# Kernel tuning notes

Measured on AMD Instinct MI355X. Metric: run time of the kernel, lower is better.

## Reference

```python
import jax, jax.numpy as jnp
import numpy as np

ALPHA = 0.2  # LeakyReLU negative slope


def setup_inputs() -> dict:
    key = jax.random.key(0)
    k1, k2, k3, k4 = jax.random.split(key, 4)
    N, E, F_IN, F_OUT = 100000, 1600000, 128, 32
    x = jax.random.normal(k1, (N, F_IN), dtype=jnp.float32)
    W = jax.random.normal(k2, (F_IN, F_OUT), dtype=jnp.float32) * 0.1
    a = jax.random.normal(k3, (2 * F_OUT, 1), dtype=jnp.float32) * 0.1
    edge_index = jax.random.randint(k4, (2, E), 0, N, dtype=jnp.int64)
    return {"x": x, "W": W, "a": a, "edge_index": edge_index}


def reference(x, W, a, edge_index):
    N = x.shape[0]
    F_OUT = W.shape[1]
    Wx = x @ W  # [N, F_OUT]
    src = edge_index[0]  # row indices (softmax groups)
    dst = edge_index[1]
    # e = leakyrelu([Wx_i || Wx_j] @ a); split a to avoid materializing the concat
    a_src = a[:F_OUT, 0]
    a_dst = a[F_OUT:, 0]
    e = (Wx @ a_src)[src] + (Wx @ a_dst)[dst]  # [E]
    e = jnp.where(e >= 0, e, ALPHA * e)
    # sparse softmax over rows (src)
    m = jax.ops.segment_max(e, src, num_segments=N)  # -inf for empty rows
    m = jnp.where(jnp.isinf(m), 0.0, m)
    exp_v = jnp.exp(e - m[src])
    s = jax.ops.segment_sum(exp_v, src, num_segments=N)
    s = jnp.where(s == 0, 1.0, s)
    att = exp_v / s[src]  # [E]
    # sparse matmul: h[i] = sum_j att[i,j] * Wx[j]
    h = jax.ops.segment_sum(att[:, None] * Wx[dst], src, num_segments=N)
    return jax.nn.elu(h)
```

## Files before the change

kernel.cpp:

```cpp
#include <hip/hip_runtime.h>
#include <hip/hip_bf16.h>
#include <math.h>

#define ALPHA 0.2f
#define F_IN 128
#define F_OUT 32
#define BSHIFT 9
#define BNODES 512
#define DSTBITS 17
#define CHUNK 4096
#define SLABCAP 16384

typedef __attribute__((ext_vector_type(8))) short short8;
typedef __attribute__((ext_vector_type(4))) float float4v;

__device__ __forceinline__ short f2bf(float f) {
    __hip_bfloat16 h = __float2bfloat16(f);
    return __builtin_bit_cast(short, h);
}
__device__ __forceinline__ float bf2f(unsigned short u) {
    return __uint_as_float((unsigned)u << 16);
}

__global__ __launch_bounds__(256) void k_phaseA(
    const float* __restrict__ x, const float* __restrict__ W,
    const float* __restrict__ a, unsigned short* __restrict__ Wxh,
    float* __restrict__ s1, float* __restrict__ s2, int nTiles, int N, int nT1,
    const int* __restrict__ src, const int* __restrict__ dst,
    int* __restrict__ bcur, unsigned* __restrict__ packed, int E)
{
    if ((int)blockIdx.x < nT1) {
        __shared__ short Wt[32 * 136];
        for (int i = threadIdx.x; i < F_IN * F_OUT; i += 256) {
            int k = i >> 5, n = i & 31;
            Wt[n * 136 + k] = f2bf(W[i]);
        }
        __syncthreads();

        int wave = threadIdx.x >> 6;
        int lane = threadIdx.x & 63;
        int tile = blockIdx.x * 4 + wave;
        if (tile >= nTiles) return;

        int m    = lane & 15;
        int quad = lane >> 4;
        int row  = tile * 16 + m;
        int rowc = row < N ? row : N - 1;

        short8 bf[2][4];
#pragma unroll
        for (int t = 0; t < 2; ++t)
#pragma unroll
            for (int s = 0; s < 4; ++s)
                bf[t][s] = *(const short8*)&Wt[(t * 16 + m) * 136 + s * 32 + quad * 8];

        float4v acc0 = {0.f, 0.f, 0.f, 0.f};
        float4v acc1 = {0.f, 0.f, 0.f, 0.f};
        const float* xr = x + (size_t)rowc * F_IN + quad * 8;
#pragma unroll
        for (int s = 0; s < 4; ++s) {
            float4 xa = *(const float4*)(xr + s * 32);
            float4 xb = *(const float4*)(xr + s * 32 + 4);
            short8 af;
            af[0] = f2bf(xa.x); af[1] = f2bf(xa.y); af[2] = f2bf(xa.z); af[3] = f2bf(xa.w);
            af[4] = f2bf(xb.x); af[5] = f2bf(xb.y); af[6] = f2bf(xb.z); af[7] = f2bf(xb.w);
            acc0 = __builtin_amdgcn_mfma_f32_16x16x32_bf16(af, bf[0][s], acc0, 0, 0, 0);
            acc1 = __builtin_amdgcn_mfma_f32_16x16x32_bf16(af, bf[1][s], acc1, 0, 0, 0);
        }

        int rbase = tile * 16 + quad * 4;
#pragma unroll
        for (int r = 0; r < 4; ++r) {
            if (rbase + r < N) {
                Wxh[(size_t)(rbase + r) * F_OUT + m]      = (unsigned short)f2bf(acc0[r]);
                Wxh[(size_t)(rbase + r) * F_OUT + m + 16] = (unsigned short)f2bf(acc1[r]);
            }
        }

        float a1c0 = a[m], a1c1 = a[m + 16];
        float a2c0 = a[F_OUT + m], a2c1 = a[F_OUT + m + 16];
#pragma unroll
        for (int r = 0; r < 4; ++r) {
            float v1 = acc0[r] * a1c0 + acc1[r] * a1c1;
            float v2 = acc0[r] * a2c0 + acc1[r] * a2c1;
#pragma unroll
            for (int off = 8; off >= 1; off >>= 1) {
                v1 += __shfl_xor(v1, off, 16);
                v2 += __shfl_xor(v2, off, 16);
            }
            if (m == 0 && rbase + r < N) {
                s1[rbase + r] = v1;
                s2[rbase + r] = v2;
            }
        }
    } else {
        __shared__ int hist[256];
        __shared__ int cur[256];
        int t = threadIdx.x;
        hist[t] = 0;
        __syncthreads();
        int e0 = ((int)blockIdx.x - nT1) * CHUNK;
        int sreg[16], dreg[16];
#pragma unroll
        for (int k = 0; k < 4; ++k) {
            int e = e0 + k * 1024 + t * 4;
            int4 s4, d4;
            if (e + 3 < E) {
                s4 = *(const int4*)&src[e];
                d4 = *(const int4*)&dst[e];
            } else {
                s4.x = (e + 0 < E) ? src[e + 0] : -1;
                s4.y = (e + 1 < E) ? src[e + 1] : -1;
                s4.z = (e + 2 < E) ? src[e + 2] : -1;
                s4.w = (e + 3 < E) ? src[e + 3] : -1;
                d4.x = (e + 0 < E) ? dst[e + 0] : 0;
                d4.y = (e + 1 < E) ? dst[e + 1] : 0;
                d4.z = (e + 2 < E) ? dst[e + 2] : 0;
                d4.w = (e + 3 < E) ? dst[e + 3] : 0;
            }
            sreg[k * 4 + 0] = s4.x; dreg[k * 4 + 0] = d4.x;
            sreg[k * 4 + 1] = s4.y; dreg[k * 4 + 1] = d4.y;
            sreg[k * 4 + 2] = s4.z; dreg[k * 4 + 2] = d4.z;
            sreg[k * 4 + 3] = s4.w; dreg[k * 4 + 3] = d4.w;
        }
#pragma unroll
        for (int k = 0; k < 16; ++k)
            if (sreg[k] >= 0) atomicAdd(&hist[sreg[k] >> BSHIFT], 1);
        __syncthreads();
        if (hist[t] > 0) cur[t] = atomicAdd(&bcur[t], hist[t]);
        __syncthreads();
#pragma unroll
        for (int k = 0; k < 16; ++k) {
            if (sreg[k] >= 0) {
                int b = sreg[k] >> BSHIFT;
                int p = atomicAdd(&cur[b], 1);
                if (p < SLABCAP)
                    packed[(size_t)b * SLABCAP + p] =
                        ((unsigned)(sreg[k] & (BNODES - 1)) << DSTBITS) | (unsigned)dreg[k];
            }
        }
    }
}

__global__ __launch_bounds__(256) void k_finalize(
    const unsigned* __restrict__ packed, const int* __restrict__ bcnt,
    int* __restrict__ counts, int* __restrict__ row_ptr,
    int* __restrict__ dst_sorted, int N, int NBK)
{
    __shared__ int hist[BNODES];
    __shared__ int psum[256];
    __shared__ int cur[BNODES];
    int b = blockIdx.x;
    int t = threadIdx.x;

    psum[t] = (t < b) ? min(bcnt[t], SLABCAP) : 0;
    __syncthreads();
    for (int off = 128; off >= 1; off >>= 1) {
        if (t < off) psum[t] += psum[t + off];
        __syncthreads();
    }
    int e0 = psum[0];
    __syncthreads();

    int cnt = min(bcnt[b], SLABCAP);
    const unsigned* pb = packed + (size_t)b * SLABCAP;

    hist[t] = 0; hist[t + 256] = 0;
    __syncthreads();
    for (int e = t; e < cnt; e += 256)
        atomicAdd(&hist[pb[e] >> DSTBITS], 1);
    __syncthreads();
    int a0 = hist[2 * t], a1 = hist[2 * t + 1];
    psum[t] = a0 + a1;
    __syncthreads();
    for (int off = 1; off < 256; off <<= 1) {
        int v = (t >= off) ? psum[t - off] : 0;
        __syncthreads();
        psum[t] += v;
        __syncthreads();
    }
    int excl = (t > 0) ? psum[t - 1] : 0;
    int p0 = e0 + excl;
    int p1 = p0 + a0;
    cur[2 * t] = p0;
    cur[2 * t + 1] = p1;
    int n0 = b << BSHIFT;
    if (n0 + 2 * t < N)     { counts[n0 + 2 * t] = a0;     row_ptr[n0 + 2 * t] = p0; }
    if (n0 + 2 * t + 1 < N) { counts[n0 + 2 * t + 1] = a1; row_ptr[n0 + 2 * t + 1] = p1; }
    __syncthreads();
    for (int e = t; e < cnt; e += 256) {
        unsigned v = pb[e];
        int p = atomicAdd(&cur[v >> DSTBITS], 1);
        dst_sorted[p] = v & ((1u << DSTBITS) - 1);
    }
}

__global__ __launch_bounds__(256) void k_node(
    const int* __restrict__ row_ptr, const int* __restrict__ counts,
    const int* __restrict__ dst_s,
    const float* __restrict__ s1, const float* __restrict__ s2,
    const unsigned short* __restrict__ Wxh, float* __restrict__ out, int N)
{
    int g = threadIdx.x >> 5;
    int l = threadIdx.x & 31;
    int n = blockIdx.x * 8 + g;
    if (n >= N) return;

    int base = row_ptr[n];
    int deg  = counts[n];
    float s1n = s1[n];
    int es = l >> 3;
    int fl = l & 7;

    float4 acc = {0.f, 0.f, 0.f, 0.f};
    float sum = 0.f;
    for (int j0 = 0; j0 < deg; j0 += 32) {
        int j = j0 + l;
        int   d_l = 0;
        float p_l = 0.f;
        if (j < deg) {
            d_l = dst_s[base + j];
            float ev = s1n + s2[d_l];
            ev = ev >= 0.f ? ev : ALPHA * ev;
            p_l = expf(ev);
        }
        sum += p_l;
        int cnt = min(32, deg - j0);
        int nIter = (cnt + 3) >> 2;
        for (int t = 0; t < nIter; ++t) {
            int e = t * 4 + es;
            float p = __shfl(p_l, e, 32);
            int   d = __shfl(d_l, e, 32);
            ushort4 w = *(const ushort4*)&Wxh[(size_t)d * F_OUT + fl * 4];
            acc.x += p * bf2f(w.x);
            acc.y += p * bf2f(w.y);
            acc.z += p * bf2f(w.z);
            acc.w += p * bf2f(w.w);
        }
    }
#pragma unroll
    for (int off = 8; off <= 16; off <<= 1) {
        acc.x += __shfl_xor(acc.x, off, 32);
        acc.y += __shfl_xor(acc.y, off, 32);
        acc.z += __shfl_xor(acc.z, off, 32);
        acc.w += __shfl_xor(acc.w, off, 32);
    }
#pragma unroll
    for (int off = 16; off >= 1; off >>= 1)
        sum += __shfl_xor(sum, off, 32);

    if (es == 0) {
        float inv = (deg > 0) ? 1.f / sum : 0.f;
        float4 h;
        h.x = acc.x * inv; h.y = acc.y * inv; h.z = acc.z * inv; h.w = acc.w * inv;
        h.x = h.x > 0.f ? h.x : expm1f(h.x);
        h.y = h.y > 0.f ? h.y : expm1f(h.y);
        h.z = h.z > 0.f ? h.z : expm1f(h.z);
        h.w = h.w > 0.f ? h.w : expm1f(h.w);
        *(float4*)&out[(size_t)n * F_OUT + fl * 4] = h;
    }
}

extern "C" void kernel_launch(void* const* d_in, const int* in_sizes, int n_in,
                              void* d_out, int out_size, void* d_ws, size_t ws_size,
                              hipStream_t stream)
{
    const float* x = (const float*)d_in[0];
    const float* W = (const float*)d_in[1];
    const float* a = (const float*)d_in[2];
    const int*  ei = (const int*)d_in[3];

    int N = in_sizes[0] / F_IN;
    int E = in_sizes[3] / 2;
    const int* src = ei;
    const int* dst = ei + E;
    int NBK = (N + BNODES - 1) >> BSHIFT;
    int nTiles = (N + 15) / 16;
    int nT1 = (nTiles + 3) / 4;
    int nEB = (E + CHUNK - 1) / CHUNK;

    unsigned short* Wxh = (unsigned short*)d_ws;
    float*    s1       = (float*)d_ws + (size_t)16 * N;
    float*    s2       = s1 + N;
    int*      counts   = (int*)(s2 + N);
    int*      row_ptr  = counts + N;
    int*      bcur     = row_ptr + N;
    unsigned* packed   = (unsigned*)(bcur + 256);
    int*      dst_sorted = (int*)(packed + (size_t)NBK * SLABCAP);

    float* out = (float*)d_out;

    hipMemsetAsync(bcur, 0, 256 * 4, stream);

    k_phaseA<<<nT1 + nEB, 256, 0, stream>>>(x, W, a, Wxh, s1, s2, nTiles, N, nT1,
                                            src, dst, bcur, packed, E);
    k_finalize<<<NBK, 256, 0, stream>>>(packed, bcur, counts, row_ptr, dst_sorted, N, NBK);
    k_node<<<(N + 7) / 8, 256, 0, stream>>>(row_ptr, counts, dst_sorted, s1, s2, Wxh, out, N);
}
```

Measured before the change: 170.6 us.

## Fuse CSR finalize and node aggregation into per-bucket LDS atomic accumulation

Shrinks source buckets from 512 to 64 nodes, which gives about 1563 buckets, and drops the finalize pass that built row_ptr and dst_sorted. A single per-bucket kernel now reads the packed edges straight from each slab, computes the exp weights, and accumulates the softmax denominator and the weighted Wx rows into shared memory with float atomics. This removes one kernel launch and a full global scatter/sort pass. In exchange it relies on contended LDS atomics, and the slab capacity of 2048 per 64-node bucket risks silently dropping edges for high-degree buckets. It also skips max-subtraction in the softmax, as the code before already did.

```diff
diff --git a/kernel.cpp b/kernel.cpp
--- a/kernel.cpp
+++ b/kernel.cpp
@@ -5,11 +5,13 @@
 #define ALPHA 0.2f
 #define F_IN 128
 #define F_OUT 32
-#define BSHIFT 9
-#define BNODES 512
+#define BSHIFT 6
+#define BNODES 64
 #define DSTBITS 17
 #define CHUNK 4096
-#define SLABCAP 16384
+#define SLABCAP 2048
+#define NBKMAX 1600
+#define ACCSTRIDE 33
 
 typedef __attribute__((ext_vector_type(8))) short short8;
 typedef __attribute__((ext_vector_type(4))) float float4v;
@@ -27,7 +29,7 @@
     const float* __restrict__ a, unsigned short* __restrict__ Wxh,
     float* __restrict__ s1, float* __restrict__ s2, int nTiles, int N, int nT1,
     const int* __restrict__ src, const int* __restrict__ dst,
-    int* __restrict__ bcur, unsigned* __restrict__ packed, int E)
+    int* __restrict__ bcur, unsigned* __restrict__ packed, int E, int NBK)
 {
     if ((int)blockIdx.x < nT1) {
         __shared__ short Wt[32 * 136];
@@ -94,10 +96,10 @@
             }
         }
     } else {
-        __shared__ int hist[256];
-        __shared__ int cur[256];
+        __shared__ int hist[NBKMAX];
+        __shared__ int cur[NBKMAX];
         int t = threadIdx.x;
-        hist[t] = 0;
+        for (int i = t; i < NBK; i += 256) hist[i] = 0;
         __syncthreads();
         int e0 = ((int)blockIdx.x - nT1) * CHUNK;
         int sreg[16], dreg[16];
@@ -127,7 +129,8 @@
         for (int k = 0; k < 16; ++k)
             if (sreg[k] >= 0) atomicAdd(&hist[sreg[k] >> BSHIFT], 1);
         __syncthreads();
-        if (hist[t] > 0) cur[t] = atomicAdd(&bcur[t], hist[t]);
+        for (int i = t; i < NBK; i += 256)
+            if (hist[i] > 0) cur[i] = atomicAdd(&bcur[i], hist[i]);
         __syncthreads();
 #pragma unroll
         for (int k = 0; k < 16; ++k) {
@@ -142,122 +145,80 @@
     }
 }
 
-__global__ __launch_bounds__(256) void k_finalize(
+__global__ __launch_bounds__(256) void k_bnode(
     const unsigned* __restrict__ packed, const int* __restrict__ bcnt,
-    int* __restrict__ counts, int* __restrict__ row_ptr,
-    int* __restrict__ dst_sorted, int N, int NBK)
-{
-    __shared__ int hist[BNODES];
-    __shared__ int psum[256];
-    __shared__ int cur[BNODES];
-    int b = blockIdx.x;
-    int t = threadIdx.x;
-
-    psum[t] = (t < b) ? min(bcnt[t], SLABCAP) : 0;
-    __syncthreads();
-    for (int off = 128; off >= 1; off >>= 1) {
-        if (t < off) psum[t] += psum[t + off];
-        __syncthreads();
-    }
-    int e0 = psum[0];
-    __syncthreads();
-
-    int cnt = min(bcnt[b], SLABCAP);
-    const unsigned* pb = packed + (size_t)b * SLABCAP;
-
-    hist[t] = 0; hist[t + 256] = 0;
-    __syncthreads();
-    for (int e = t; e < cnt; e += 256)
-        atomicAdd(&hist[pb[e] >> DSTBITS], 1);
-    __syncthreads();
-    int a0 = hist[2 * t], a1 = hist[2 * t + 1];
-    psum[t] = a0 + a1;
-    __syncthreads();
-    for (int off = 1; off < 256; off <<= 1) {
-        int v = (t >= off) ? psum[t - off] : 0;
-        __syncthreads();
-        psum[t] += v;
-        __syncthreads();
-    }
-    int excl = (t > 0) ? psum[t - 1] : 0;
-    int p0 = e0 + excl;
-    int p1 = p0 + a0;
-    cur[2 * t] = p0;
-    cur[2 * t + 1] = p1;
-    int n0 = b << BSHIFT;
-    if (n0 + 2 * t < N)     { counts[n0 + 2 * t] = a0;     row_ptr[n0 + 2 * t] = p0; }
-    if (n0 + 2 * t + 1 < N) { counts[n0 + 2 * t + 1] = a1; row_ptr[n0 + 2 * t + 1] = p1; }
-    __syncthreads();
-    for (int e = t; e < cnt; e += 256) {
-        unsigned v = pb[e];
-        int p = atomicAdd(&cur[v >> DSTBITS], 1);
-        dst_sorted[p] = v & ((1u << DSTBITS) - 1);
-    }
-}
-
-__global__ __launch_bounds__(256) void k_node(
-    const int* __restrict__ row_ptr, const int* __restrict__ counts,
-    const int* __restrict__ dst_s,
     const float* __restrict__ s1, const float* __restrict__ s2,
     const unsigned short* __restrict__ Wxh, float* __restrict__ out, int N)
 {
-    int g = threadIdx.x >> 5;
-    int l = threadIdx.x & 31;
-    int n = blockIdx.x * 8 + g;
-    if (n >= N) return;
-
-    int base = row_ptr[n];
-    int deg  = counts[n];
-    float s1n = s1[n];
-    int es = l >> 3;
-    int fl = l & 7;
-
-    float4 acc = {0.f, 0.f, 0.f, 0.f};
-    float sum = 0.f;
-    for (int j0 = 0; j0 < deg; j0 += 32) {
-        int j = j0 + l;
-        int   d_l = 0;
+    __shared__ float acc[BNODES * ACCSTRIDE];
+    __shared__ float denom[BNODES];
+    __shared__ float s1l[BNODES];
+    int b = blockIdx.x;
+    int t = threadIdx.x;
+    int n0 = b << BSHIFT;
+
+    for (int i = t; i < BNODES * ACCSTRIDE; i += 256) acc[i] = 0.f;
+    if (t < BNODES) {
+        denom[t] = 0.f;
+        int n = n0 + t;
+        s1l[t] = (n < N) ? s1[n] : 0.f;
+    }
+    __syncthreads();
+
+    int cnt = min(bcnt[b], SLABCAP);
+    const unsigned* pb = packed + (size_t)b * SLABCAP;
+
+    int lane = t & 63;
+    int es = lane >> 3;
+    int fl = lane & 7;
+
+    for (int j0 = 0; j0 < cnt; j0 += 256) {
+        int j = j0 + t;
+        int ls_l = 0, d_l = 0;
         float p_l = 0.f;
-        if (j < deg) {
-            d_l = dst_s[base + j];
-            float ev = s1n + s2[d_l];
+        if (j < cnt) {
+            unsigned v = pb[j];
+            ls_l = v >> DSTBITS;
+            d_l  = v & ((1u << DSTBITS) - 1);
+            float ev = s1l[ls_l] + s2[d_l];
             ev = ev >= 0.f ? ev : ALPHA * ev;
             p_l = expf(ev);
-        }
-        sum += p_l;
-        int cnt = min(32, deg - j0);
-        int nIter = (cnt + 3) >> 2;
-        for (int t = 0; t < nIter; ++t) {
-            int e = t * 4 + es;
-            float p = __shfl(p_l, e, 32);
-            int   d = __shfl(d_l, e, 32);
+            atomicAdd(&denom[ls_l], p_l);
+        }
+        int base = j0 + (t & ~63);
+        int m = cnt - base;
+        if (m > 64) m = 64;
+        int nIter = (m + 7) >> 3;
+        for (int it = 0; it < nIter; ++it) {
+            int e = it * 8 + es;
+            float p  = __shfl(p_l, e, 64);
+            int   d  = __shfl(d_l, e, 64);
+            int   ls = __shfl(ls_l, e, 64);
             ushort4 w = *(const ushort4*)&Wxh[(size_t)d * F_OUT + fl * 4];
-            acc.x += p * bf2f(w.x);
-            acc.y += p * bf2f(w.y);
-            acc.z += p * bf2f(w.z);
-            acc.w += p * bf2f(w.w);
-        }
-    }
-#pragma unroll
-    for (int off = 8; off <= 16; off <<= 1) {
-        acc.x += __shfl_xor(acc.x, off, 32);
-        acc.y += __shfl_xor(acc.y, off, 32);
-        acc.z += __shfl_xor(acc.z, off, 32);
-        acc.w += __shfl_xor(acc.w, off, 32);
-    }
-#pragma unroll
-    for (int off = 16; off >= 1; off >>= 1)
-        sum += __shfl_xor(sum, off, 32);
-
-    if (es == 0) {
-        float inv = (deg > 0) ? 1.f / sum : 0.f;
-        float4 h;
-        h.x = acc.x * inv; h.y = acc.y * inv; h.z = acc.z * inv; h.w = acc.w * inv;
-        h.x = h.x > 0.f ? h.x : expm1f(h.x);
-        h.y = h.y > 0.f ? h.y : expm1f(h.y);
-        h.z = h.z > 0.f ? h.z : expm1f(h.z);
-        h.w = h.w > 0.f ? h.w : expm1f(h.w);
-        *(float4*)&out[(size_t)n * F_OUT + fl * 4] = h;
+            float* ap = &acc[ls * ACCSTRIDE + fl * 4];
+            atomicAdd(ap + 0, p * bf2f(w.x));
+            atomicAdd(ap + 1, p * bf2f(w.y));
+            atomicAdd(ap + 2, p * bf2f(w.z));
+            atomicAdd(ap + 3, p * bf2f(w.w));
+        }
+    }
+    __syncthreads();
+
+    for (int i = t; i < BNODES * (F_OUT / 4); i += 256) {
+        int ls = i >> 3, fq = i & 7;
+        int n = n0 + ls;
+        if (n < N) {
+            float dn = denom[ls];
+            float inv = dn > 0.f ? 1.f / dn : 0.f;
+            const float* ap = &acc[ls * ACCSTRIDE + fq * 4];
+            float4 h;
+            h.x = ap[0] * inv; h.y = ap[1] * inv; h.z = ap[2] * inv; h.w = ap[3] * inv;
+            h.x = h.x > 0.f ? h.x : expm1f(h.x);
+            h.y = h.y > 0.f ? h.y : expm1f(h.y);
+            h.z = h.z > 0.f ? h.z : expm1f(h.z);
+            h.w = h.w > 0.f ? h.w : expm1f(h.w);
+            *(float4*)&out[(size_t)n * F_OUT + fq * 4] = h;
+        }
     }
 }
 
@@ -282,18 +243,14 @@
     unsigned short* Wxh = (unsigned short*)d_ws;
     float*    s1       = (float*)d_ws + (size_t)16 * N;
     float*    s2       = s1 + N;
-    int*      counts   = (int*)(s2 + N);
-    int*      row_ptr  = counts + N;
-    int*      bcur     = row_ptr + N;
-    unsigned* packed   = (unsigned*)(bcur + 256);
-    int*      dst_sorted = (int*)(packed + (size_t)NBK * SLABCAP);
+    int*      bcur     = (int*)(s2 + N);
+    unsigned* packed   = (unsigned*)(bcur + NBKMAX);
 
     float* out = (float*)d_out;
 
-    hipMemsetAsync(bcur, 0, 256 * 4, stream);
+    hipMemsetAsync(bcur, 0, (size_t)NBK * 4, stream);
 
     k_phaseA<<<nT1 + nEB, 256, 0, stream>>>(x, W, a, Wxh, s1, s2, nTiles, N, nT1,
-                                            src, dst, bcur, packed, E);
-    k_finalize<<<NBK, 256, 0, stream>>>(packed, bcur, counts, row_ptr, dst_sorted, N, NBK);
-    k_node<<<(N + 7) / 8, 256, 0, stream>>>(row_ptr, counts, dst_sorted, s1, s2, Wxh, out, N);
-}
+                                            src, dst, bcur, packed, E, NBK);
+    k_bnode<<<NBK, 256, 0, stream>>>(packed, bcur, s1, s2, Wxh, out, N);
+}
```

After: 437.7 us. +156.6%, slower.

## Fuse per-bucket CSR finalize into node aggregation kernel with LDS-resident sorting

Applied to the files above, without the earlier changes.

Shrinks buckets to 128 nodes (782 buckets) and merges the finalize and node kernels into one kernel. Each block sorts its bucket's packed edges in shared memory and then aggregates its nodes directly, so the dst_sorted, row_ptr and counts global round trips and one launch go away. In exchange the aggregation grid drops to about 782 blocks, each looping over 16 nodes per group, which may lower parallelism and occupancy. The fixed slab cap of 3072 edges per bucket silently drops edges in buckets above that size.

```diff
diff --git a/kernel.cpp b/kernel.cpp
--- a/kernel.cpp
+++ b/kernel.cpp
@@ -5,11 +5,13 @@
 #define ALPHA 0.2f
 #define F_IN 128
 #define F_OUT 32
-#define BSHIFT 9
-#define BNODES 512
+#define BSHIFT 7
+#define BNODES 128
 #define DSTBITS 17
-#define CHUNK 4096
-#define SLABCAP 16384
+#define CHUNK 2048
+#define SLABCAP 3072
+#define NBKMAX 800
+#define MAXPER 12
 
 typedef __attribute__((ext_vector_type(8))) short short8;
 typedef __attribute__((ext_vector_type(4))) float float4v;
@@ -27,7 +29,7 @@
     const float* __restrict__ a, unsigned short* __restrict__ Wxh,
     float* __restrict__ s1, float* __restrict__ s2, int nTiles, int N, int nT1,
     const int* __restrict__ src, const int* __restrict__ dst,
-    int* __restrict__ bcur, unsigned* __restrict__ packed, int E)
+    int* __restrict__ bcur, unsigned* __restrict__ packed, int E, int NBK)
 {
     if ((int)blockIdx.x < nT1) {
         __shared__ short Wt[32 * 136];
@@ -94,15 +96,15 @@
             }
         }
     } else {
-        __shared__ int hist[256];
-        __shared__ int cur[256];
+        __shared__ int hist[NBKMAX];
+        __shared__ int cur[NBKMAX];
         int t = threadIdx.x;
-        hist[t] = 0;
+        for (int i = t; i < NBK; i += 256) hist[i] = 0;
         __syncthreads();
         int e0 = ((int)blockIdx.x - nT1) * CHUNK;
-        int sreg[16], dreg[16];
-#pragma unroll
-        for (int k = 0; k < 4; ++k) {
+        int sreg[8], dreg[8];
+#pragma unroll
+        for (int k = 0; k < 2; ++k) {
             int e = e0 + k * 1024 + t * 4;
             int4 s4, d4;
             if (e + 3 < E) {
@@ -124,13 +126,14 @@
             sreg[k * 4 + 3] = s4.w; dreg[k * 4 + 3] = d4.w;
         }
 #pragma unroll
-        for (int k = 0; k < 16; ++k)
+        for (int k = 0; k < 8; ++k)
             if (sreg[k] >= 0) atomicAdd(&hist[sreg[k] >> BSHIFT], 1);
         __syncthreads();
-        if (hist[t] > 0) cur[t] = atomicAdd(&bcur[t], hist[t]);
-        __syncthreads();
-#pragma unroll
-        for (int k = 0; k < 16; ++k) {
+        for (int i = t; i < NBK; i += 256)
+            if (hist[i] > 0) cur[i] = atomicAdd(&bcur[i], hist[i]);
+        __syncthreads();
+#pragma unroll
+        for (int k = 0; k < 8; ++k) {
             if (sreg[k] >= 0) {
                 int b = sreg[k] >> BSHIFT;
                 int p = atomicAdd(&cur[b], 1);
@@ -142,122 +145,130 @@
     }
 }
 
-__global__ __launch_bounds__(256) void k_finalize(
+__global__ __launch_bounds__(256) void k_bnode(
     const unsigned* __restrict__ packed, const int* __restrict__ bcnt,
-    int* __restrict__ counts, int* __restrict__ row_ptr,
-    int* __restrict__ dst_sorted, int N, int NBK)
-{
-    __shared__ int hist[BNODES];
-    __shared__ int psum[256];
-    __shared__ int cur[BNODES];
-    int b = blockIdx.x;
-    int t = threadIdx.x;
-
-    psum[t] = (t < b) ? min(bcnt[t], SLABCAP) : 0;
-    __syncthreads();
-    for (int off = 128; off >= 1; off >>= 1) {
-        if (t < off) psum[t] += psum[t + off];
-        __syncthreads();
-    }
-    int e0 = psum[0];
-    __syncthreads();
-
-    int cnt = min(bcnt[b], SLABCAP);
-    const unsigned* pb = packed + (size_t)b * SLABCAP;
-
-    hist[t] = 0; hist[t + 256] = 0;
-    __syncthreads();
-    for (int e = t; e < cnt; e += 256)
-        atomicAdd(&hist[pb[e] >> DSTBITS], 1);
-    __syncthreads();
-    int a0 = hist[2 * t], a1 = hist[2 * t + 1];
-    psum[t] = a0 + a1;
-    __syncthreads();
-    for (int off = 1; off < 256; off <<= 1) {
-        int v = (t >= off) ? psum[t - off] : 0;
-        __syncthreads();
-        psum[t] += v;
-        __syncthreads();
-    }
-    int excl = (t > 0) ? psum[t - 1] : 0;
-    int p0 = e0 + excl;
-    int p1 = p0 + a0;
-    cur[2 * t] = p0;
-    cur[2 * t + 1] = p1;
-    int n0 = b << BSHIFT;
-    if (n0 + 2 * t < N)     { counts[n0 + 2 * t] = a0;     row_ptr[n0 + 2 * t] = p0; }
-    if (n0 + 2 * t + 1 < N) { counts[n0 + 2 * t + 1] = a1; row_ptr[n0 + 2 * t + 1] = p1; }
-    __syncthreads();
-    for (int e = t; e < cnt; e += 256) {
-        unsigned v = pb[e];
-        int p = atomicAdd(&cur[v >> DSTBITS], 1);
-        dst_sorted[p] = v & ((1u << DSTBITS) - 1);
-    }
-}
-
-__global__ __launch_bounds__(256) void k_node(
-    const int* __restrict__ row_ptr, const int* __restrict__ counts,
-    const int* __restrict__ dst_s,
     const float* __restrict__ s1, const float* __restrict__ s2,
     const unsigned short* __restrict__ Wxh, float* __restrict__ out, int N)
 {
-    int g = threadIdx.x >> 5;
-    int l = threadIdx.x & 31;
-    int n = blockIdx.x * 8 + g;
-    if (n >= N) return;
-
-    int base = row_ptr[n];
-    int deg  = counts[n];
-    float s1n = s1[n];
+    __shared__ unsigned sorted[SLABCAP];
+    __shared__ int psum[256];
+    __shared__ int rpl[BNODES];
+    __shared__ int degl[BNODES];
+    __shared__ int cur[BNODES];
+    __shared__ int histl[BNODES];
+    __shared__ float s1l[BNODES];
+
+    int b = blockIdx.x;
+    int t = threadIdx.x;
+    int n0 = b << BSHIFT;
+    int cnt = min(bcnt[b], SLABCAP);
+    const unsigned* pb = packed + (size_t)b * SLABCAP;
+
+    if (t < BNODES) {
+        histl[t] = 0;
+        int n = n0 + t;
+        s1l[t] = (n < N) ? s1[n] : 0.f;
+    }
+    __syncthreads();
+
+    unsigned ereg[MAXPER];
+#pragma unroll
+    for (int k = 0; k < MAXPER; ++k) {
+        int j = k * 256 + t;
+        ereg[k] = (j < cnt) ? pb[j] : 0xFFFFFFFFu;
+    }
+#pragma unroll
+    for (int k = 0; k < MAXPER; ++k)
+        if (ereg[k] != 0xFFFFFFFFu) atomicAdd(&histl[ereg[k] >> DSTBITS], 1);
+    __syncthreads();
+
+    int a0 = (t < BNODES) ? histl[t] : 0;
+    psum[t] = a0;
+    __syncthreads();
+    for (int off = 1; off < BNODES; off <<= 1) {
+        int v = (t >= off) ? psum[t - off] : 0;
+        __syncthreads();
+        psum[t] += v;
+        __syncthreads();
+    }
+    if (t < BNODES) {
+        int excl = (t > 0) ? psum[t - 1] : 0;
+        rpl[t] = excl;
+        cur[t] = excl;
+        degl[t] = a0;
+    }
+    __syncthreads();
+
+#pragma unroll
+    for (int k = 0; k < MAXPER; ++k) {
+        if (ereg[k] != 0xFFFFFFFFu) {
+            int ls = ereg[k] >> DSTBITS;
+            int p = atomicAdd(&cur[ls], 1);
+            sorted[p] = ereg[k];
+        }
+    }
+    __syncthreads();
+
+    int g = t >> 5;
+    int l = t & 31;
     int es = l >> 3;
     int fl = l & 7;
 
-    float4 acc = {0.f, 0.f, 0.f, 0.f};
-    float sum = 0.f;
-    for (int j0 = 0; j0 < deg; j0 += 32) {
-        int j = j0 + l;
-        int   d_l = 0;
-        float p_l = 0.f;
-        if (j < deg) {
-            d_l = dst_s[base + j];
-            float ev = s1n + s2[d_l];
-            ev = ev >= 0.f ? ev : ALPHA * ev;
-            p_l = expf(ev);
-        }
-        sum += p_l;
-        int cnt = min(32, deg - j0);
-        int nIter = (cnt + 3) >> 2;
-        for (int t = 0; t < nIter; ++t) {
-            int e = t * 4 + es;
-            float p = __shfl(p_l, e, 32);
-            int   d = __shfl(d_l, e, 32);
-            ushort4 w = *(const ushort4*)&Wxh[(size_t)d * F_OUT + fl * 4];
-            acc.x += p * bf2f(w.x);
-            acc.y += p * bf2f(w.y);
-            acc.z += p * bf2f(w.z);
-            acc.w += p * bf2f(w.w);
-        }
-    }
-#pragma unroll
-    for (int off = 8; off <= 16; off <<= 1) {
-        acc.x += __shfl_xor(acc.x, off, 32);
-        acc.y += __shfl_xor(acc.y, off, 32);
-        acc.z += __shfl_xor(acc.z, off, 32);
-        acc.w += __shfl_xor(acc.w, off, 32);
-    }
-#pragma unroll
-    for (int off = 16; off >= 1; off >>= 1)
-        sum += __shfl_xor(sum, off, 32);
-
-    if (es == 0) {
-        float inv = (deg > 0) ? 1.f / sum : 0.f;
-        float4 h;
-        h.x = acc.x * inv; h.y = acc.y * inv; h.z = acc.z * inv; h.w = acc.w * inv;
-        h.x = h.x > 0.f ? h.x : expm1f(h.x);
-        h.y = h.y > 0.f ? h.y : expm1f(h.y);
-        h.z = h.z > 0.f ? h.z : expm1f(h.z);
-        h.w = h.w > 0.f ? h.w : expm1f(h.w);
-        *(float4*)&out[(size_t)n * F_OUT + fl * 4] = h;
+    for (int ni = 0; ni < BNODES / 8; ++ni) {
+        int ls = g * (BNODES / 8) + ni;
+        int n = n0 + ls;
+        if (n >= N) break;
+        int base = rpl[ls];
+        int deg  = degl[ls];
+        float s1n = s1l[ls];
+
+        float4 acc = {0.f, 0.f, 0.f, 0.f};
+        float sum = 0.f;
+        for (int j0 = 0; j0 < deg; j0 += 32) {
+            int j = j0 + l;
+            int   d_l = 0;
+            float p_l = 0.f;
+            if (j < deg) {
+                d_l = (int)(sorted[base + j] & ((1u << DSTBITS) - 1));
+                float ev = s1n + s2[d_l];
+                ev = ev >= 0.f ? ev : ALPHA * ev;
+                p_l = expf(ev);
+            }
+            sum += p_l;
+            int cnt2 = min(32, deg - j0);
+            int nIter = (cnt2 + 3) >> 2;
+            for (int it = 0; it < nIter; ++it) {
+                int e = it * 4 + es;
+                float p = __shfl(p_l, e, 32);
+                int   d = __shfl(d_l, e, 32);
+                ushort4 w = *(const ushort4*)&Wxh[(size_t)d * F_OUT + fl * 4];
+                acc.x += p * bf2f(w.x);
+                acc.y += p * bf2f(w.y);
+                acc.z += p * bf2f(w.z);
+                acc.w += p * bf2f(w.w);
+            }
+        }
+#pragma unroll
+        for (int off = 8; off <= 16; off <<= 1) {
+            acc.x += __shfl_xor(acc.x, off, 32);
+            acc.y += __shfl_xor(acc.y, off, 32);
+            acc.z += __shfl_xor(acc.z, off, 32);
+            acc.w += __shfl_xor(acc.w, off, 32);
+        }
+#pragma unroll
+        for (int off = 16; off >= 1; off >>= 1)
+            sum += __shfl_xor(sum, off, 32);
+
+        if (es == 0) {
+            float inv = (deg > 0) ? 1.f / sum : 0.f;
+            float4 h;
+            h.x = acc.x * inv; h.y = acc.y * inv; h.z = acc.z * inv; h.w = acc.w * inv;
+            h.x = h.x > 0.f ? h.x : expm1f(h.x);
+            h.y = h.y > 0.f ? h.y : expm1f(h.y);
+            h.z = h.z > 0.f ? h.z : expm1f(h.z);
+            h.w = h.w > 0.f ? h.w : expm1f(h.w);
+            *(float4*)&out[(size_t)n * F_OUT + fl * 4] = h;
+        }
     }
 }
 
@@ -282,18 +293,14 @@
     unsigned short* Wxh = (unsigned short*)d_ws;
     float*    s1       = (float*)d_ws + (size_t)16 * N;
     float*    s2       = s1 + N;
-    int*      counts   = (int*)(s2 + N);
-    int*      row_ptr  = counts + N;
-    int*      bcur     = row_ptr + N;
-    unsigned* packed   = (unsigned*)(bcur + 256);
-    int*      dst_sorted = (int*)(packed + (size_t)NBK * SLABCAP);
+    int*      bcur     = (int*)(s2 + N);
+    unsigned* packed   = (unsigned*)(bcur + NBKMAX);
 
     float* out = (float*)d_out;
 
-    hipMemsetAsync(bcur, 0, 256 * 4, stream);
+    hipMemsetAsync(bcur, 0, (size_t)NBK * 4, stream);
 
     k_phaseA<<<nT1 + nEB, 256, 0, stream>>>(x, W, a, Wxh, s1, s2, nTiles, N, nT1,
-                                            src, dst, bcur, packed, E);
-    k_finalize<<<NBK, 256, 0, stream>>>(packed, bcur, counts, row_ptr, dst_sorted, N, NBK);
-    k_node<<<(N + 7) / 8, 256, 0, stream>>>(row_ptr, counts, dst_sorted, s1, s2, Wxh, out, N);
-}
+                                            src, dst, bcur, packed, E, NBK);
+    k_bnode<<<NBK, 256, 0, stream>>>(packed, bcur, s1, s2, Wxh, out, N);
+}
```

Measured after the change: 180.3 us. +5.7%, slower.
